# Kernel tuning notes

Hardware: AMD Instinct MI355X
Metric: run time of the kernel (lower is better)

Reference implementation:

```python
import jax, jax.numpy as jnp
import numpy as np

# R2D2-style NghSampler2 config
NGH, SUBQ, SUBD, POS_D, NEG_D, BORDER, SUBD_NEG = 7, 8, 1, 3, 5, 16, 8

def _make_offsets():
    rad = (NGH // SUBD) * NGH
    pos, neg = [], []
    for j in range(-rad, rad + 1, SUBD):
        for i in range(-rad, rad + 1, SUBD):
            d2 = i * i + j * j
            if d2 <= POS_D ** 2:
                pos.append((i, j))
            elif NEG_D ** 2 <= d2 <= NGH ** 2:
                neg.append((i, j))
    # rows: [x(i), y(j)], matching torch .view(-1,2).t()
    return np.array(pos, np.int32).T, np.array(neg, np.int32).T

POS_OFF, NEG_OFF = _make_offsets()  # [2,29], [2,80]

def _grid(B, H, W, step):
    xs = np.arange(BORDER, W - BORDER, step)
    ys = np.arange(BORDER, H - BORDER, step)
    H1, W1 = len(ys), len(xs)
    b1 = np.repeat(np.arange(B), H1 * W1)
    y1 = np.tile(np.repeat(ys, W1), B)
    x1 = np.tile(np.tile(xs, H1), B)
    return b1, y1, x1, (B, H1, W1)

def setup_inputs() -> dict:
    key = jax.random.key(0)
    k1, k2, k3, k4, k5 = jax.random.split(key, 5)
    B, C, H, W = 4, 128, 256, 256
    feat1 = jax.random.normal(k1, (B, C, H, W), jnp.float32)
    feat2 = jax.random.normal(k2, (B, C, H, W), jnp.float32)
    conf1 = jax.random.uniform(k3, (B, 1, H, W), jnp.float32)
    conf2 = jax.random.uniform(k4, (B, 1, H, W), jnp.float32)
    aflow = jax.random.uniform(k5, (B, 2, H, W), jnp.float32) * (W - 1)
    return {"feat1": feat1, "feat2": feat2, "conf1": conf1, "conf2": conf2, "aflow": aflow}

def reference(feat1, feat2, conf1, conf2, aflow):
    B, C, H, W = feat1.shape
    b1n, y1n, x1n, shape = _grid(B, H, W, SUBQ)
    b1, y1, x1 = jnp.asarray(b1n), jnp.asarray(y1n), jnp.asarray(x1n)
    pos_off, neg_off = jnp.asarray(POS_OFF), jnp.asarray(NEG_OFF)

    f1 = feat1[b1, :, y1, x1]                      # [Q,C] query descriptors
    qconf = conf1[b1, 0, y1, x1].reshape(shape)    # [B,H1,W1]
    xy2 = (aflow[b1, :, y1, x1] + 0.5).astype(jnp.int32).T  # [2,Q] (x,y)
    mask = ((xy2[0] >= 0) & (xy2[1] >= 0) & (xy2[0] < W) & (xy2[1] < H)).reshape(shape)

    def clamp(xy):
        return jnp.stack([jnp.clip(xy[0], 0, W - 1), jnp.clip(xy[1], 0, H - 1)])

    # positives: gather feat2 at GT-correspondence + pos offsets, dot with f1
    xy2p = clamp(xy2[:, None, :] + pos_off[:, :, None])      # [2,P,Q]
    f2p = feat2[b1, :, xy2p[1], xy2p[0]]                     # [P,Q,C]
    ps_all = jnp.einsum('qc,pqc->qp', f1, f2p)               # [Q,P]
    pscores = ps_all.max(axis=1, keepdims=True)              # [Q,1]
    pos = jnp.argmax(ps_all, axis=1)                         # [Q]
    sel = clamp(xy2 + pos_off[:, pos])                       # [2,Q]
    qconf = (qconf + conf2[b1, 0, sel[1], sel[0]].reshape(shape)) / 2

    # negatives: ring of offsets around GT correspondence
    xy2n = clamp(xy2[:, None, :] + neg_off[:, :, None])      # [2,N,Q]
    f2n = feat2[b1, :, xy2n[1], xy2n[0]]                     # [N,Q,C]
    nscores = jnp.einsum('qc,nqc->qn', f1, f2n)              # [Q,N]

    # distractors on a regular grid in image 2
    b3n, y3n, x3n, _ = _grid(B, H, W, SUBD_NEG)
    b3, y3, x3 = jnp.asarray(b3n), jnp.asarray(y3n), jnp.asarray(x3n)
    distractors = feat2[b3, :, y3, x3]                       # [Q2,C]
    dscores = f1 @ distractors.T                             # [Q,Q2]
    dis2 = (x3[None, :] - xy2[0][:, None]) ** 2 \
         + (y3[None, :] - xy2[1][:, None]) ** 2 \
         + (b3[None, :] != b1[:, None]).astype(jnp.int32) * NEG_D ** 2
    dscores = jnp.where(dis2 < NEG_D ** 2, 0.0, dscores)

    scores = jnp.concatenate([pscores, nscores, dscores], axis=1)
    npos = pscores.shape[1]
    gt = jnp.concatenate([
        jnp.ones((scores.shape[0], npos), jnp.uint8),
        jnp.zeros((scores.shape[0], scores.shape[1] - npos), jnp.uint8)], axis=1)
    return scores, gt, mask, qconf
```

## Files before the change

### kernel.cpp

```cpp
#include <hip/hip_runtime.h>

#define CCH   128
#define HH    256
#define WW    256
#define BB    4
#define H1    28
#define W1    28
#define QTOT  3136
#define NPOS  29
#define NNEG  80
#define NDIS  3136
#define DT64  (NDIS / 64)
#define QT64  (QTOT / 64)
#define SCOLS 3217

typedef short s8v __attribute__((ext_vector_type(8)));
typedef float f4v __attribute__((ext_vector_type(4)));
typedef float f4raw __attribute__((ext_vector_type(4)));
typedef unsigned int u2v __attribute__((ext_vector_type(2)));

__device__ __forceinline__ unsigned short f2bf(float f) {
  unsigned int u = __float_as_uint(f);
  u += 0x7fffu + ((u >> 16) & 1u);
  return (unsigned short)(u >> 16);
}
__device__ __forceinline__ float bflo(unsigned int v) { return __uint_as_float(v << 16); }
__device__ __forceinline__ float bfhi(unsigned int v) { return __uint_as_float(v & 0xffff0000u); }

__constant__ int POS_I[NPOS] = {
  0, -2,-1,0,1,2, -2,-1,0,1,2, -3,-2,-1,0,1,2,3, -2,-1,0,1,2, -2,-1,0,1,2, 0};
__constant__ int POS_J[NPOS] = {
  -3, -2,-2,-2,-2,-2, -1,-1,-1,-1,-1, 0,0,0,0,0,0,0, 1,1,1,1,1, 2,2,2,2,2, 3};
__constant__ int NEG_I[NNEG] = {
  0, -3,-2,-1,0,1,2,3, -4,-3,-2,-1,0,1,2,3,4, -5,-4,-3,3,4,5, -6,-5,-4,4,5,6,
  -6,-5,5,6, -6,-5,5,6, -7,-6,-5,5,6,7, -6,-5,5,6, -6,-5,5,6, -6,-5,-4,4,5,6,
  -5,-4,-3,3,4,5, -4,-3,-2,-1,0,1,2,3,4, -3,-2,-1,0,1,2,3, 0};
__constant__ int NEG_J[NNEG] = {
  -7, -6,-6,-6,-6,-6,-6,-6, -5,-5,-5,-5,-5,-5,-5,-5,-5, -4,-4,-4,-4,-4,-4,
  -3,-3,-3,-3,-3,-3, -2,-2,-2,-2, -1,-1,-1,-1, 0,0,0,0,0,0, 1,1,1,1, 2,2,2,2,
  3,3,3,3,3,3, 4,4,4,4,4,4, 5,5,5,5,5,5,5,5,5, 6,6,6,6,6,6,6, 7};

__global__ __launch_bounds__(256, 6)
void transpose_kernel(const float* __restrict__ feat2,
                      const float* __restrict__ feat1,
                      const float* __restrict__ aflow,
                      unsigned short* __restrict__ feat2T,
                      unsigned short* __restrict__ F1bf,
                      unsigned short* __restrict__ F2bf,
                      int* __restrict__ X2, int* __restrict__ Y2,
                      float* __restrict__ mask_out) {
  __shared__ __align__(16) unsigned int tile[2][32][66];

  int x0 = blockIdx.x * 32;
  int y0 = blockIdx.y * 2;
  int b  = blockIdx.z;
  int tid = threadIdx.x;
  int cp = tid >> 3;
  int xq = tid & 7;

  const float* fbase = feat2 + (size_t)b * CCH * HH * WW;
  f4raw v[2][2][2];
  #pragma unroll
  for (int r = 0; r < 2; ++r)
    #pragma unroll
    for (int h = 0; h < 2; ++h) {
      int c0 = 2 * (h * 32 + cp);
      const float* p = fbase + ((size_t)c0 * HH + (y0 + r)) * WW + x0 + 4 * xq;
      v[r][h][0] = __builtin_nontemporal_load((const f4raw*)p);
      v[r][h][1] = __builtin_nontemporal_load((const f4raw*)(p + (size_t)HH * WW));
    }

  #pragma unroll
  for (int r = 0; r < 2; ++r)
    #pragma unroll
    for (int h = 0; h < 2; ++h) {
      int cpf = h * 32 + cp;
      f4raw a = v[r][h][0], c = v[r][h][1];
      tile[r][4 * xq + 0][cpf] = (unsigned)f2bf(a.x) | ((unsigned)f2bf(c.x) << 16);
      tile[r][4 * xq + 1][cpf] = (unsigned)f2bf(a.y) | ((unsigned)f2bf(c.y) << 16);
      tile[r][4 * xq + 2][cpf] = (unsigned)f2bf(a.z) | ((unsigned)f2bf(c.z) << 16);
      tile[r][4 * xq + 3][cpf] = (unsigned)f2bf(a.w) | ((unsigned)f2bf(c.w) << 16);
    }
  __syncthreads();

  int xi = tid >> 3;
  int cg = (tid & 7) * 8;
  #pragma unroll
  for (int r = 0; r < 2; ++r) {
    u2v t0 = *(const u2v*)&tile[r][xi][cg + 0];
    u2v t1 = *(const u2v*)&tile[r][xi][cg + 2];
    u2v t2 = *(const u2v*)&tile[r][xi][cg + 4];
    u2v t3 = *(const u2v*)&tile[r][xi][cg + 6];
    unsigned int* dst = (unsigned int*)(feat2T +
        ((size_t)((b * HH + y0 + r) * WW) + x0 + xi) * CCH) + cg;
    ((uint4*)dst)[0] = make_uint4(t0.x, t0.y, t1.x, t1.y);
    ((uint4*)dst)[1] = make_uint4(t2.x, t2.y, t3.x, t3.y);
  }

  #pragma unroll
  for (int r = 0; r < 2; ++r) {
    int y = y0 + r;
    if ((y & 7) == 0 && y >= 16 && y <= 232) {
      int xs = x0 + (tid >> 6) * 8;
      if (xs >= 16 && xs <= 232) {
        int cpq = tid & 63;
        int q = b * H1 * W1 + ((y - 16) >> 3) * W1 + ((xs - 16) >> 3);
        ((unsigned int*)(F2bf + (size_t)q * CCH))[cpq] = tile[r][xs - x0][cpq];
        const float* f1p = feat1 + ((size_t)(b * CCH + 2 * cpq) * HH + y) * WW + xs;
        unsigned int l1 = f2bf(f1p[0]);
        unsigned int h1 = f2bf(f1p[(size_t)HH * WW]);
        ((unsigned int*)(F1bf + (size_t)q * CCH))[cpq] = l1 | (h1 << 16);
        if (cpq == 0) {
          float ax = aflow[((size_t)(b * 2 + 0) * HH + y) * WW + xs];
          float ay = aflow[((size_t)(b * 2 + 1) * HH + y) * WW + xs];
          int px = (int)(ax + 0.5f);
          int py = (int)(ay + 0.5f);
          X2[q] = px; Y2[q] = py;
          mask_out[q] = (px >= 0 && py >= 0 && px < WW && py < HH) ? 1.0f : 0.0f;
        }
      }
    }
  }
}

__global__ void main_kernel(const unsigned short* __restrict__ feat2T,
                            const float* __restrict__ conf1,
                            const float* __restrict__ conf2,
                            const unsigned short* __restrict__ F1bf,
                            const unsigned short* __restrict__ F2bf,
                            const int* __restrict__ X2, const int* __restrict__ Y2,
                            float* __restrict__ scores, float* __restrict__ gt,
                            float* __restrict__ qconf_out) {
  __shared__ union {
    struct { float tile[64][66]; int sx2[64]; int sy2[64]; } ds;
    struct { __align__(16) float f1s[CCH]; float posv[NPOS]; float negv[NNEG];
             float bestv; } pn;
  } sm;

  if (blockIdx.x < QTOT) {
    int q = blockIdx.x, t = threadIdx.x;
    int b = q / (H1 * W1), r = q % (H1 * W1);
    int y = 16 + 8 * (r / W1);
    int x = 16 + 8 * (r % W1);

    if (t < 64) {
      unsigned int u = ((const unsigned int*)(F1bf + (size_t)q * CCH))[t];
      sm.pn.f1s[2 * t]     = bflo(u);
      sm.pn.f1s[2 * t + 1] = bfhi(u);
    }
    int x2 = X2[q], y2 = Y2[q];
    __syncthreads();

    if (t < 2 * (NPOS + NNEG)) {
      int off = t >> 1, half = t & 1;
      int di = (off < NPOS) ? POS_I[off] : NEG_I[off - NPOS];
      int dj = (off < NPOS) ? POS_J[off] : NEG_J[off - NPOS];
      int xk = min(max(x2 + di, 0), WW - 1);
      int yk = min(max(y2 + dj, 0), HH - 1);
      const uint4* p4 = (const uint4*)(feat2T +
          ((size_t)((b * HH + yk) * WW) + xk) * CCH + half * 64);
      float acc = 0.f;
      #pragma unroll
      for (int i = 0; i < 8; ++i) {
        uint4 v = p4[i];
        float4 fa = *(const float4*)&sm.pn.f1s[half * 64 + i * 8];
        float4 fb = *(const float4*)&sm.pn.f1s[half * 64 + i * 8 + 4];
        acc += fa.x * bflo(v.x) + fa.y * bfhi(v.x)
             + fa.z * bflo(v.y) + fa.w * bfhi(v.y)
             + fb.x * bflo(v.z) + fb.y * bfhi(v.z)
             + fb.z * bflo(v.w) + fb.w * bfhi(v.w);
      }
      acc += __shfl_xor(acc, 1);
      if (half == 0) {
        if (off < NPOS) sm.pn.posv[off] = acc;
        else            sm.pn.negv[off - NPOS] = acc;
      }
    }
    if (t < 1 + NNEG)
      gt[(size_t)q * SCOLS + t] = (t == 0) ? 1.0f : 0.0f;
    __syncthreads();

    if (t == 0) {
      float best = sm.pn.posv[0]; int bi = 0;
      for (int k = 1; k < NPOS; ++k)
        if (sm.pn.posv[k] > best) { best = sm.pn.posv[k]; bi = k; }
      sm.pn.bestv = best;
      int sx = min(max(x2 + POS_I[bi], 0), WW - 1);
      int sy = min(max(y2 + POS_J[bi], 0), HH - 1);
      float c1 = conf1[((size_t)b * HH + y) * WW + x];
      float c2 = conf2[((size_t)b * HH + sy) * WW + sx];
      qconf_out[q] = 0.5f * (c1 + c2);
    }
    __syncthreads();

    if (t < 1 + NNEG)
      scores[(size_t)q * SCOLS + t] = (t == 0) ? sm.pn.bestv : sm.pn.negv[t - 1];

  } else {
    int bid = blockIdx.x - QTOT;
    int qb = (bid / DT64) * 64;
    int db = (bid % DT64) * 64;
    int w = threadIdx.x >> 6, lane = threadIdx.x & 63;
    int m  = lane & 15;
    int ko = (lane >> 4) * 8;

    if (threadIdx.x < 64) {
      sm.ds.sx2[threadIdx.x] = X2[qb + threadIdx.x];
      sm.ds.sy2[threadIdx.x] = Y2[qb + threadIdx.x];
    }

    f4v acc[4];
    #pragma unroll
    for (int dt = 0; dt < 4; ++dt) acc[dt] = (f4v){0.f, 0.f, 0.f, 0.f};

    #pragma unroll
    for (int kk = 0; kk < 4; ++kk) {
      s8v a = *(const s8v*)(F1bf + (size_t)(qb + w * 16 + m) * CCH + kk * 32 + ko);
      #pragma unroll
      for (int dt = 0; dt < 4; ++dt) {
        s8v bfr = *(const s8v*)(F2bf + (size_t)(db + dt * 16 + m) * CCH + kk * 32 + ko);
        acc[dt] = __builtin_amdgcn_mfma_f32_16x16x32_bf16(a, bfr, acc[dt], 0, 0, 0);
      }
    }

    int rbase = (lane >> 4) * 4, col = lane & 15;
    #pragma unroll
    for (int dt = 0; dt < 4; ++dt)
      #pragma unroll
      for (int r = 0; r < 4; ++r)
        sm.ds.tile[w * 16 + rbase + r][dt * 16 + col] = acc[dt][r];
    __syncthreads();

    int d = db + lane;
    int dbat = d / (H1 * W1), dr = d % (H1 * W1);
    int dy = 16 + 8 * (dr / W1), dx = 16 + 8 * (dr % W1);

    #pragma unroll
    for (int i = 0; i < 16; ++i) {
      int row = w * 16 + i;
      int q = qb + row;
      int qbat = q / (H1 * W1);
      int ddx = dx - sm.ds.sx2[row], ddy = dy - sm.ds.sy2[row];
      int dis2 = ddx * ddx + ddy * ddy + (dbat != qbat ? 25 : 0);
      float v = sm.ds.tile[row][lane];
      if (dis2 < 25) v = 0.f;
      size_t o = (size_t)q * SCOLS + 1 + NNEG + d;
      __builtin_nontemporal_store(v,   &scores[o]);
      __builtin_nontemporal_store(0.f, &gt[o]);
    }
  }
}

extern "C" void kernel_launch(void* const* d_in, const int* in_sizes, int n_in,
                              void* d_out, int out_size, void* d_ws, size_t ws_size,
                              hipStream_t stream) {
  const float* feat1 = (const float*)d_in[0];
  const float* feat2 = (const float*)d_in[1];
  const float* conf1 = (const float*)d_in[2];
  const float* conf2 = (const float*)d_in[3];
  const float* aflow = (const float*)d_in[4];

  float* out       = (float*)d_out;
  float* scores    = out;
  float* gt        = out + (size_t)QTOT * SCOLS;
  float* mask_out  = out + 2 * (size_t)QTOT * SCOLS;
  float* qconf_out = mask_out + QTOT;

  unsigned short* feat2T = (unsigned short*)d_ws;
  unsigned short* F1bf   = feat2T + (size_t)BB * HH * WW * CCH;
  unsigned short* F2bf   = F1bf + (size_t)QTOT * CCH;
  int* X2 = (int*)(F2bf + (size_t)QTOT * CCH);
  int* Y2 = X2 + QTOT;

  dim3 gT(WW / 32, HH / 2, BB);
  transpose_kernel<<<gT, 256, 0, stream>>>(feat2, feat1, aflow, feat2T,
                                           F1bf, F2bf, X2, Y2, mask_out);
  main_kernel<<<QTOT + DT64 * QT64, 256, 0, stream>>>(feat2T, conf1, conf2,
                                                      F1bf, F2bf, X2, Y2,
                                                      scores, gt, qconf_out);
}
```

Baseline: 337.3 us.

## Vectorize distractor score stores to float4 and parallelize positive argmax

```diff
diff --git a/kernel.cpp b/kernel.cpp
--- a/kernel.cpp
+++ b/kernel.cpp
@@ -17,6 +17,7 @@
 typedef short s8v __attribute__((ext_vector_type(8)));
 typedef float f4v __attribute__((ext_vector_type(4)));
 typedef float f4raw __attribute__((ext_vector_type(4)));
+typedef float f4u __attribute__((ext_vector_type(4), aligned(4)));
 typedef unsigned int u2v __attribute__((ext_vector_type(2)));
 
 __device__ __forceinline__ unsigned short f2bf(float f) {
@@ -132,7 +133,7 @@
                             float* __restrict__ scores, float* __restrict__ gt,
                             float* __restrict__ qconf_out) {
   __shared__ union {
-    struct { float tile[64][66]; int sx2[64]; int sy2[64]; } ds;
+    struct { __align__(16) float tile[64][68]; int sx2[64]; int sy2[64]; } ds;
     struct { __align__(16) float f1s[CCH]; float posv[NPOS]; float negv[NNEG];
              float bestv; } pn;
   } sm;
@@ -180,16 +181,23 @@
       gt[(size_t)q * SCOLS + t] = (t == 0) ? 1.0f : 0.0f;
     __syncthreads();
 
-    if (t == 0) {
-      float best = sm.pn.posv[0]; int bi = 0;
-      for (int k = 1; k < NPOS; ++k)
-        if (sm.pn.posv[k] > best) { best = sm.pn.posv[k]; bi = k; }
-      sm.pn.bestv = best;
-      int sx = min(max(x2 + POS_I[bi], 0), WW - 1);
-      int sy = min(max(y2 + POS_J[bi], 0), HH - 1);
-      float c1 = conf1[((size_t)b * HH + y) * WW + x];
-      float c2 = conf2[((size_t)b * HH + sy) * WW + sx];
-      qconf_out[q] = 0.5f * (c1 + c2);
+    if (t < 32) {
+      float bv = (t < NPOS) ? sm.pn.posv[t] : -3.4e38f;
+      int bi = t;
+      #pragma unroll
+      for (int s = 16; s; s >>= 1) {
+        float ov = __shfl_xor(bv, s);
+        int oi = __shfl_xor(bi, s);
+        if (ov > bv || (ov == bv && oi < bi)) { bv = ov; bi = oi; }
+      }
+      if (t == 0) {
+        sm.pn.bestv = bv;
+        int sx = min(max(x2 + POS_I[bi], 0), WW - 1);
+        int sy = min(max(y2 + POS_J[bi], 0), HH - 1);
+        float c1 = conf1[((size_t)b * HH + y) * WW + x];
+        float c2 = conf2[((size_t)b * HH + sy) * WW + sx];
+        qconf_out[q] = 0.5f * (c1 + c2);
+      }
     }
     __syncthreads();
 
@@ -231,22 +239,33 @@
         sm.ds.tile[w * 16 + rbase + r][dt * 16 + col] = acc[dt][r];
     __syncthreads();
 
-    int d = db + lane;
-    int dbat = d / (H1 * W1), dr = d % (H1 * W1);
-    int dy = 16 + 8 * (dr / W1), dx = 16 + 8 * (dr % W1);
-
-    #pragma unroll
-    for (int i = 0; i < 16; ++i) {
-      int row = w * 16 + i;
+    int col4  = (threadIdx.x & 15) * 4;
+    int rslot = threadIdx.x >> 4;
+    int dxs[4], dys[4], dbats[4];
+    #pragma unroll
+    for (int k = 0; k < 4; ++k) {
+      int d = db + col4 + k;
+      int dbat = d / (H1 * W1), dr = d % (H1 * W1);
+      dys[k] = 16 + 8 * (dr / W1);
+      dxs[k] = 16 + 8 * (dr % W1);
+      dbats[k] = dbat;
+    }
+    #pragma unroll
+    for (int p = 0; p < 4; ++p) {
+      int row = p * 16 + rslot;
       int q = qb + row;
       int qbat = q / (H1 * W1);
-      int ddx = dx - sm.ds.sx2[row], ddy = dy - sm.ds.sy2[row];
-      int dis2 = ddx * ddx + ddy * ddy + (dbat != qbat ? 25 : 0);
-      float v = sm.ds.tile[row][lane];
-      if (dis2 < 25) v = 0.f;
-      size_t o = (size_t)q * SCOLS + 1 + NNEG + d;
-      __builtin_nontemporal_store(v,   &scores[o]);
-      __builtin_nontemporal_store(0.f, &gt[o]);
+      int sx = sm.ds.sx2[row], sy = sm.ds.sy2[row];
+      f4raw vv = *(const f4raw*)&sm.ds.tile[row][col4];
+      #pragma unroll
+      for (int k = 0; k < 4; ++k) {
+        int ddx = dxs[k] - sx, ddy = dys[k] - sy;
+        int dis2 = ddx * ddx + ddy * ddy + (dbats[k] != qbat ? 25 : 0);
+        if (dis2 < 25) vv[k] = 0.f;
+      }
+      size_t o = (size_t)q * SCOLS + 1 + NNEG + db + col4;
+      __builtin_nontemporal_store(vv, (f4u*)&scores[o]);
+      __builtin_nontemporal_store((f4u){0.f, 0.f, 0.f, 0.f}, (f4u*)&gt[o]);
     }
   }
 }
```

Measured after the change: 346.1 us. 2.6% more time.
